# Performance work log

Measured on AMD Instinct MI355X. Metric: run time of the kernel, lower is better.

## Reference

```python
import jax, jax.numpy as jnp
import numpy as np

NEG = -1e20
EPS = float(np.finfo(np.float32).eps)


def setup_inputs() -> dict:
    key = jax.random.key(0)
    k1, k2, k3, k4 = jax.random.split(key, 4)
    B, S, E, D = 8, 2048, 1024, 1024
    return {
        "embeddings": jax.random.normal(k1, (B, S, E), dtype=jnp.float32),
        "mask": jnp.ones((B, S), dtype=jnp.int32),
        "W_q": jax.random.normal(k2, (E, D), dtype=jnp.float32),
        "W_k": jax.random.normal(k3, (E, D), dtype=jnp.float32),
        "W_v": jax.random.normal(k4, (E, D), dtype=jnp.float32),
    }


def reference(embeddings, mask, W_q, W_k, W_v):
    # embeddings: [B,S,E]; mask: [B,S] (1 = keep, 0 = pad)
    q = embeddings @ W_q            # [B,S,D]
    k = embeddings @ W_k            # [B,S,D]
    v = embeddings @ W_v            # [B,S,Dv]
    energy = jnp.einsum("bqd,bkd->bqk", q, k)  # [B,S,S]
    S = embeddings.shape[1]
    causal = jnp.tril(jnp.ones((S, S), dtype=bool))          # [S,S]
    energy = jnp.where(causal[None, :, :], energy, NEG)
    pad = (mask == 0)[:, None, :]                             # [B,1,S]
    energy = jnp.where(pad, NEG, energy)
    d_k = jnp.float32(W_k.shape[1])
    scale = jnp.sqrt(d_k) + EPS
    attention = jax.nn.softmax(energy / scale, axis=-1)       # [B,S,S]
    output = jnp.einsum("bqk,bkd->bqd", attention, v)         # [B,S,Dv]
    return output, attention
```

## Files before the change

kernel.cpp:

```cpp
#include <hip/hip_runtime.h>

#define Bb 8
#define Ss 2048
#define Ee 1024
#define Dd 1024

typedef __attribute__((ext_vector_type(8))) __bf16 bf16x8;
typedef __attribute__((ext_vector_type(4))) float f32x4;
typedef unsigned short u16;

__device__ __forceinline__ u16 f2bf(float x) {
  unsigned u = __float_as_uint(x);
  return (u16)((u + 0x7fffu + ((u >> 16) & 1u)) >> 16);
}
__device__ __forceinline__ float bf2f(u16 h) {
  return __uint_as_float(((unsigned)h) << 16);
}

__device__ __forceinline__ void gload16(const void* g, void* l) {
  __builtin_amdgcn_global_load_lds(
      (__attribute__((address_space(1))) void*)const_cast<void*>(g),
      (__attribute__((address_space(3))) void*)l, 16, 0, 0);
}

#define MFMA_BF16 __builtin_amdgcn_mfma_f32_16x16x32_bf16

__global__ __launch_bounds__(256) void k_split4(const float* __restrict__ in,
                                                u16* __restrict__ hi,
                                                u16* __restrict__ lo,
                                                long long n4) {
  long long i = (long long)blockIdx.x * 256 + threadIdx.x;
  if (i >= n4) return;
  float4 v = ((const float4*)in)[i];
  float xs[4] = {v.x, v.y, v.z, v.w};
  u16 hh[4], ll[4];
#pragma unroll
  for (int j = 0; j < 4; ++j) {
    hh[j] = f2bf(xs[j]);
    ll[j] = f2bf(xs[j] - bf2f(hh[j]));
  }
  ushort4 h, l;
  h.x = hh[0]; h.y = hh[1]; h.z = hh[2]; h.w = hh[3];
  l.x = ll[0]; l.y = ll[1]; l.z = ll[2]; l.w = ll[3];
  ((ushort4*)hi)[i] = h;
  ((ushort4*)lo)[i] = l;
}

__global__ __launch_bounds__(256) void k_wt_split(const float* __restrict__ W,
                                                  u16* __restrict__ hi,
                                                  u16* __restrict__ lo) {
  __shared__ float t[32][33];
  const int tx = threadIdx.x & 31;
  const int ty = threadIdx.x >> 5;
  const int e0 = blockIdx.y * 32, d0 = blockIdx.x * 32;
#pragma unroll
  for (int r = ty; r < 32; r += 8)
    t[r][tx] = W[(long long)(e0 + r) * Dd + d0 + tx];
  __syncthreads();
#pragma unroll
  for (int r = ty; r < 32; r += 8) {
    float x = t[tx][r];
    long long o = (long long)(d0 + r) * Ee + e0 + tx;
    u16 h = f2bf(x);
    hi[o] = h;
    if (lo) lo[o] = f2bf(x - bf2f(h));
  }
}

template <int EPI, bool CAUSAL>
__global__ __launch_bounds__(512, 4) void k_g128(
    const u16* __restrict__ Ah, const u16* __restrict__ Al,
    const u16* __restrict__ Bh, const u16* __restrict__ Bl,
    float* __restrict__ Cf, u16* __restrict__ Ch, u16* __restrict__ Cl,
    int nbx, int N, int K, long long strOp, long long strC) {
  const int nwg = gridDim.x;
  const int f = blockIdx.x;
  const int wgid = (f & 7) * (nwg >> 3) + (f >> 3);
  int bx, by, bz;
  if (CAUSAL) {
    bz = wgid / 136;
    const int t = wgid % 136;
    int yy = 0, c = 0;
    while (c + yy + 1 <= t) { c += yy + 1; ++yy; }
    by = yy;
    bx = t - c;
  } else {
    bz = 0;
    bx = wgid % nbx;
    by = wgid / nbx;
  }

  __shared__ __align__(16) u16 lds[2][4][4096];

  const int tid = threadIdx.x;
  const int lane = tid & 63;
  const int w = tid >> 6;
  const int wr = w >> 1;
  const int wc = w & 1;

  const long long ob = (long long)bz * strOp;
  const u16* srcBase[4] = {Ah + ob, Al + ob, Bh + ob, Bl + ob};
  const long long row0[2] = {(long long)by * 128, (long long)bx * 128};

  const int rL = tid >> 2;
  const int colOff = ((tid & 3) ^ ((tid >> 3) & 3)) * 8;
  const int rdOff = (lane & 15) * 64 + ((((lane >> 4) & 3) ^ ((lane >> 1) & 3)) << 4);

  const int AR = wr * 32;
  const int BR = wc * 64;
  const int nt = K / 32;

  const u16* gp[4];
#pragma unroll
  for (int m = 0; m < 4; ++m)
    gp[m] = srcBase[m] + (row0[m >> 1] + rL) * (long long)K + colOff;

#define STG(BUF)                                                       \
  {                                                                    \
    _Pragma("unroll") for (int m = 0; m < 4; ++m) {                    \
      gload16(gp[m], (char*)&lds[BUF][m][0] + tid * 16);               \
      gp[m] += 32;                                                     \
    }                                                                  \
  }
#define LDFRAG(MAT, R) \
  (*(const bf16x8*)((const char*)&lds[cur][MAT][0] + (R)*64 + rdOff))
#define BAR __builtin_amdgcn_s_barrier()

#define CLUSTER(NH)                                                          \
  __builtin_amdgcn_s_setprio(1);                                             \
  _Pragma("unroll") for (int m = 0; m < 2; ++m)                              \
      _Pragma("unroll") for (int n = 0; n < 2; ++n)                          \
          acc[m][(NH)*2 + n] =                                               \
      MFMA_BF16(aH[m], bL[n], acc[m][(NH)*2 + n], 0, 0, 0);                  \
  _Pragma("unroll") for (int m = 0; m < 2; ++m)                              \
      _Pragma("unroll") for (int n = 0; n < 2; ++n)                          \
          acc[m][(NH)*2 + n] =                                               \
      MFMA_BF16(aL[m], bH[n], acc[m][(NH)*2 + n], 0, 0, 0);                  \
  _Pragma("unroll") for (int m = 0; m < 2; ++m)                              \
      _Pragma("unroll") for (int n = 0; n < 2; ++n)                          \
          acc[m][(NH)*2 + n] =                                               \
      MFMA_BF16(aH[m], bH[n], acc[m][(NH)*2 + n], 0, 0, 0);                  \
  __builtin_amdgcn_s_setprio(0);

  f32x4 acc[2][4];
#pragma unroll
  for (int m = 0; m < 2; ++m)
#pragma unroll
    for (int n = 0; n < 4; ++n) acc[m][n] = f32x4{0.f, 0.f, 0.f, 0.f};

  bf16x8 aH[2], aL[2], bH[2], bL[2];

  STG(0);

  for (int kt = 0; kt < nt; ++kt) {
    const int cur = kt & 1;
    const bool more = (kt + 1 < nt);

    if (more) {
      STG(cur ^ 1);
      asm volatile("s_waitcnt vmcnt(4)" ::: "memory");
    } else {
      asm volatile("s_waitcnt vmcnt(0)" ::: "memory");
    }
    BAR;

#pragma unroll
    for (int m = 0; m < 2; ++m) {
      aH[m] = LDFRAG(0, AR + m * 16);
      aL[m] = LDFRAG(1, AR + m * 16);
    }
#pragma unroll
    for (int n = 0; n < 2; ++n) {
      bH[n] = LDFRAG(2, BR + n * 16);
      bL[n] = LDFRAG(3, BR + n * 16);
    }
    BAR;
    CLUSTER(0);
    BAR;

#pragma unroll
    for (int n = 0; n < 2; ++n) {
      bH[n] = LDFRAG(2, BR + 32 + n * 16);
      bL[n] = LDFRAG(3, BR + 32 + n * 16);
    }
    BAR;
    CLUSTER(1);
    BAR;
  }

  const int cr = (lane >> 4) << 2;
  const int cc = lane & 15;
#pragma unroll
  for (int m = 0; m < 2; ++m)
#pragma unroll
    for (int n = 0; n < 4; ++n)
#pragma unroll
      for (int r = 0; r < 4; ++r) {
        const long long row = (long long)by * 128 + wr * 32 + m * 16 + cr + r;
        const long long col = (long long)bx * 128 + wc * 64 + n * 16 + cc;
        const float v = acc[m][n][r];
        if constexpr (EPI == 0) {
          Cf[(long long)bz * strC + row * N + col] = v;
        } else {
          const long long idx = row * N + col;
          u16 h = f2bf(v);
          Ch[idx] = h;
          Cl[idx] = f2bf(v - bf2f(h));
        }
      }
#undef STG
#undef LDFRAG
#undef BAR
#undef CLUSTER
}

template <int EPI, bool TRIK>
__global__ __launch_bounds__(256) void k_gemm_bt(
    const u16* __restrict__ Ah, const u16* __restrict__ Bh,
    float* __restrict__ Cf, u16* __restrict__ Ch,
    int M, int N, int K, long long strA, long long strB, long long strC) {
  const int bx = blockIdx.x, by = blockIdx.y, bz = blockIdx.z;

  const int tid = threadIdx.x;
  const int lane = tid & 63;
  const int w = tid >> 6;
  const int wr = w >> 1, wc = w & 1;

  const u16* pAh = Ah + (long long)bz * strA;
  const u16* pBh = Bh + (long long)bz * strB;

  __shared__ __align__(16) u16 lds[2 * 128 * 32];
  char* ldsc = (char*)lds;

  const int srow = tid >> 2;
  const int scol = (tid & 3) * 8;
  const long long arow = (long long)by * 128 + srow;
  const long long brow = (long long)bx * 128 + srow;

  int ktEnd = K / 32;
  if (TRIK) {
    int lim = ((by + 1) * 128) / 32;
    if (lim < ktEnd) ktEnd = lim;
  }

  f32x4 acc[4][4];
#pragma unroll
  for (int i = 0; i < 4; ++i)
#pragma unroll
    for (int j = 0; j < 4; ++j) acc[i][j] = f32x4{0.f, 0.f, 0.f, 0.f};

  for (int kt = 0; kt < ktEnd; ++kt) {
    const int k0 = kt * 32 + scol;
    __syncthreads();
    gload16(pAh + arow * K + k0, ldsc + 0 * 4096 + w * 1024);
    gload16(pAh + (arow + 64) * K + k0, ldsc + 1 * 4096 + w * 1024);
    gload16(pBh + brow * K + k0, ldsc + 8192 + 0 * 4096 + w * 1024);
    gload16(pBh + (brow + 64) * K + k0, ldsc + 8192 + 1 * 4096 + w * 1024);
    __syncthreads();

    const int kk = (lane >> 4) * 8;
    const int ar = wr * 64 + (lane & 15);
    const int br = wc * 64 + (lane & 15);
    bf16x8 avh[4], bvh[4];
#pragma unroll
    for (int m = 0; m < 4; ++m)
      avh[m] = *(const bf16x8*)(lds + (ar + m * 16) * 32 + kk);
#pragma unroll
    for (int n = 0; n < 4; ++n)
      bvh[n] = *(const bf16x8*)(lds + 128 * 32 + (br + n * 16) * 32 + kk);
#pragma unroll
    for (int m = 0; m < 4; ++m)
#pragma unroll
      for (int n = 0; n < 4; ++n)
        acc[m][n] = MFMA_BF16(avh[m], bvh[n], acc[m][n], 0, 0, 0);
  }

  const int cr = wr * 64 + ((lane >> 4) << 2);
  const int cc = wc * 64 + (lane & 15);
  const long long rb = (long long)by * 128 + cr;
  const long long cb = (long long)bx * 128 + cc;
#pragma unroll
  for (int m = 0; m < 4; ++m)
#pragma unroll
    for (int n = 0; n < 4; ++n)
#pragma unroll
      for (int r = 0; r < 4; ++r) {
        const long long idx =
            (long long)bz * strC + (rb + m * 16 + r) * (long long)N + (cb + n * 16);
        const float v = acc[m][n][r];
        if constexpr (EPI == 0) Cf[idx] = v;
        else Ch[idx] = f2bf(v);
      }
}

__global__ __launch_bounds__(256) void k_softmax(float* __restrict__ attn,
                                                 u16* __restrict__ attn_bf,
                                                 const int* __restrict__ mask,
                                                 float inv_scale) {
  const int q = blockIdx.x;
  const int b = blockIdx.y;
  const int tid = threadIdx.x;
  float* row = attn + ((long long)b * Ss + q) * Ss;
  u16* rowb = attn_bf + ((long long)b * Ss + q) * Ss;
  const int* mrow = mask + b * Ss;
  const int qup = ((q >> 7) + 1) << 7;

  float x[8];
  float m = -3.0e38f;
#pragma unroll
  for (int j = 0; j < 8; ++j) {
    const int k = tid + j * 256;
    float v = -3.0e38f;
    if (k <= q) {
      const float e = row[k];
      v = ((mrow[k] != 0) ? e : -1e20f) * inv_scale;
    }
    x[j] = v;
    m = fmaxf(m, v);
  }
#pragma unroll
  for (int o = 32; o > 0; o >>= 1) m = fmaxf(m, __shfl_xor(m, o));
  __shared__ float redm[4], reds[4];
  const int w = tid >> 6;
  if ((tid & 63) == 0) redm[w] = m;
  __syncthreads();
  m = fmaxf(fmaxf(redm[0], redm[1]), fmaxf(redm[2], redm[3]));
  float s = 0.f;
#pragma unroll
  for (int j = 0; j < 8; ++j) {
    x[j] = __expf(x[j] - m);
    s += x[j];
  }
#pragma unroll
  for (int o = 32; o > 0; o >>= 1) s += __shfl_xor(s, o);
  if ((tid & 63) == 0) reds[w] = s;
  __syncthreads();
  s = reds[0] + reds[1] + reds[2] + reds[3];
  const float inv = 1.0f / s;
#pragma unroll
  for (int j = 0; j < 8; ++j) {
    const int k = tid + j * 256;
    if (k <= q) {
      const float a = x[j] * inv;
      row[k] = a;
      rowb[k] = f2bf(a);
    } else {
      row[k] = 0.0f;
      if (k < qup) rowb[k] = 0;
    }
  }
}

extern "C" void kernel_launch(void* const* d_in, const int* in_sizes, int n_in,
                              void* d_out, int out_size, void* d_ws, size_t ws_size,
                              hipStream_t stream) {
  const float* emb = (const float*)d_in[0];
  const int* mask = (const int*)d_in[1];
  const float* Wq = (const float*)d_in[2];
  const float* Wk = (const float*)d_in[3];
  const float* Wv = (const float*)d_in[4];

  float* out = (float*)d_out;
  float* attn = out + (long long)Bb * Ss * Dd;

  char* p = (char*)d_ws;
  u16* emb_hi = (u16*)p;
  u16* emb_lo = emb_hi + 16777216LL;
  u16* R_hi = (u16*)(p + 67108864LL);
  u16* R_lo = R_hi + 16777216LL;
  u16* v_t = R_lo + 16777216LL;
  u16* attn_bf = v_t + 16777216LL;
  u16* Wqr_hi = attn_bf + 16777216LL;
  u16* Wqr_lo = Wqr_hi + 1048576LL;
  u16* Wkr_hi = Wqr_lo + 1048576LL;
  u16* Wkr_lo = Wkr_hi + 1048576LL;
  u16* M_hi = Wkr_lo + 1048576LL;
  u16* M_lo = M_hi + 1048576LL;
  u16* WvT_hi = M_lo + 1048576LL;

  const float inv_scale = 1.0f / (32.0f + 1.1920929e-07f);

  k_split4<<<16384, 256, 0, stream>>>(emb, emb_hi, emb_lo, 4194304LL);
  k_split4<<<1024, 256, 0, stream>>>(Wq, Wqr_hi, Wqr_lo, 262144LL);
  k_split4<<<1024, 256, 0, stream>>>(Wk, Wkr_hi, Wkr_lo, 262144LL);
  k_wt_split<<<dim3(32, 32), 256, 0, stream>>>(Wv, WvT_hi, nullptr);

  k_g128<1, false><<<64, 512, 0, stream>>>(
      Wkr_hi, Wkr_lo, Wqr_hi, Wqr_lo, nullptr, M_hi, M_lo, 8, 1024, 1024, 0, 0);
  k_g128<1, false><<<1024, 512, 0, stream>>>(
      emb_hi, emb_lo, M_hi, M_lo, nullptr, R_hi, R_lo, 8, 1024, 1024, 0, 0);
  k_gemm_bt<2, false><<<dim3(16, 8, 8), 256, 0, stream>>>(
      WvT_hi, emb_hi, nullptr, v_t,
      1024, 2048, 1024, 0, (long long)Ss * Ee, (long long)Dd * Ss);
  k_g128<0, true><<<1088, 512, 0, stream>>>(
      R_hi, R_lo, emb_hi, emb_lo, attn, nullptr, nullptr,
      0, Ss, Dd, (long long)Ss * Dd, (long long)Ss * Ss);
  k_softmax<<<dim3(Ss, Bb), 256, 0, stream>>>(attn, attn_bf, mask, inv_scale);
  k_gemm_bt<0, true><<<dim3(8, 16, 8), 256, 0, stream>>>(
      attn_bf, v_t, out, nullptr,
      2048, 1024, 2048, (long long)Ss * Ss, (long long)Dd * Ss, (long long)Ss * Dd);
}
```

Baseline: 486.8 us.

## Replace simple bf16 GEMM with double-buffered 512-thread tile kernel for V and PV

Generalizes the double-buffered 128x128 tile kernel with a single-precision-pass mode: two bf16 operands instead of hi/lo pairs, optional batching through blockIdx.y, and triangular K limiting. It replaces the old 256-thread GEMM, which reloaded LDS behind two full barriers every K step with no prefetch, for the V projection and the attention-times-V product. The goal is to overlap global-to-LDS loads with MFMA work and to gain from the swizzled block ordering. The trade-off is a smaller per-wave output tile (32x64) and more barriers per iteration in the new path.

```diff
diff --git a/kernel.cpp b/kernel.cpp
--- a/kernel.cpp
+++ b/kernel.cpp
@@ -67,12 +67,13 @@
   }
 }
 
-template <int EPI, bool CAUSAL>
-__global__ __launch_bounds__(512, 4) void k_g128(
+template <int NP, int EPI, bool CAUSAL, bool TRIK>
+__global__ __launch_bounds__(512, 4) void k_t128(
     const u16* __restrict__ Ah, const u16* __restrict__ Al,
     const u16* __restrict__ Bh, const u16* __restrict__ Bl,
     float* __restrict__ Cf, u16* __restrict__ Ch, u16* __restrict__ Cl,
-    int nbx, int N, int K, long long strOp, long long strC) {
+    int nbx, int N, int K, long long strA, long long strB, long long strC) {
+  constexpr int NMAT = (NP == 3) ? 4 : 2;
   const int nwg = gridDim.x;
   const int f = blockIdx.x;
   const int wgid = (f & 7) * (nwg >> 3) + (f >> 3);
@@ -85,12 +86,12 @@
     by = yy;
     bx = t - c;
   } else {
-    bz = 0;
+    bz = blockIdx.y;
     bx = wgid % nbx;
     by = wgid / nbx;
   }
 
-  __shared__ __align__(16) u16 lds[2][4][4096];
+  __shared__ __align__(16) u16 lds[2][NMAT][4096];
 
   const int tid = threadIdx.x;
   const int lane = tid & 63;
@@ -98,8 +99,16 @@
   const int wr = w >> 1;
   const int wc = w & 1;
 
-  const long long ob = (long long)bz * strOp;
-  const u16* srcBase[4] = {Ah + ob, Al + ob, Bh + ob, Bl + ob};
+  const u16* srcBase[NMAT];
+  if constexpr (NP == 3) {
+    srcBase[0] = Ah + (long long)bz * strA;
+    srcBase[1] = Al + (long long)bz * strA;
+    srcBase[2] = Bh + (long long)bz * strB;
+    srcBase[3] = Bl + (long long)bz * strB;
+  } else {
+    srcBase[0] = Ah + (long long)bz * strA;
+    srcBase[1] = Bh + (long long)bz * strB;
+  }
   const long long row0[2] = {(long long)by * 128, (long long)bx * 128};
 
   const int rL = tid >> 2;
@@ -108,16 +117,22 @@
 
   const int AR = wr * 32;
   const int BR = wc * 64;
-  const int nt = K / 32;
-
-  const u16* gp[4];
-#pragma unroll
-  for (int m = 0; m < 4; ++m)
-    gp[m] = srcBase[m] + (row0[m >> 1] + rL) * (long long)K + colOff;
+  int nt = K / 32;
+  if (TRIK) {
+    const int lim = ((by + 1) * 128) / 32;
+    if (lim < nt) nt = lim;
+  }
+
+  const u16* gp[NMAT];
+#pragma unroll
+  for (int m = 0; m < NMAT; ++m) {
+    const int opsel = (NP == 3) ? (m >> 1) : m;
+    gp[m] = srcBase[m] + (row0[opsel] + rL) * (long long)K + colOff;
+  }
 
 #define STG(BUF)                                                       \
   {                                                                    \
-    _Pragma("unroll") for (int m = 0; m < 4; ++m) {                    \
+    _Pragma("unroll") for (int m = 0; m < NMAT; ++m) {                 \
       gload16(gp[m], (char*)&lds[BUF][m][0] + tid * 16);               \
       gp[m] += 32;                                                     \
     }                                                                  \
@@ -126,7 +141,7 @@
   (*(const bf16x8*)((const char*)&lds[cur][MAT][0] + (R)*64 + rdOff))
 #define BAR __builtin_amdgcn_s_barrier()
 
-#define CLUSTER(NH)                                                          \
+#define CLUSTER3(NH)                                                         \
   __builtin_amdgcn_s_setprio(1);                                             \
   _Pragma("unroll") for (int m = 0; m < 2; ++m)                              \
       _Pragma("unroll") for (int n = 0; n < 2; ++n)                          \
@@ -149,6 +164,7 @@
     for (int n = 0; n < 4; ++n) acc[m][n] = f32x4{0.f, 0.f, 0.f, 0.f};
 
   bf16x8 aH[2], aL[2], bH[2], bL[2];
+  bf16x8 bF[4];
 
   STG(0);
 
@@ -158,34 +174,52 @@
 
     if (more) {
       STG(cur ^ 1);
-      asm volatile("s_waitcnt vmcnt(4)" ::: "memory");
+      if constexpr (NP == 3)
+        asm volatile("s_waitcnt vmcnt(4)" ::: "memory");
+      else
+        asm volatile("s_waitcnt vmcnt(2)" ::: "memory");
     } else {
       asm volatile("s_waitcnt vmcnt(0)" ::: "memory");
     }
     BAR;
 
-#pragma unroll
-    for (int m = 0; m < 2; ++m) {
-      aH[m] = LDFRAG(0, AR + m * 16);
-      aL[m] = LDFRAG(1, AR + m * 16);
+    if constexpr (NP == 3) {
+#pragma unroll
+      for (int m = 0; m < 2; ++m) {
+        aH[m] = LDFRAG(0, AR + m * 16);
+        aL[m] = LDFRAG(1, AR + m * 16);
+      }
+#pragma unroll
+      for (int n = 0; n < 2; ++n) {
+        bH[n] = LDFRAG(2, BR + n * 16);
+        bL[n] = LDFRAG(3, BR + n * 16);
+      }
+      BAR;
+      CLUSTER3(0);
+      BAR;
+#pragma unroll
+      for (int n = 0; n < 2; ++n) {
+        bH[n] = LDFRAG(2, BR + 32 + n * 16);
+        bL[n] = LDFRAG(3, BR + 32 + n * 16);
+      }
+      BAR;
+      CLUSTER3(1);
+      BAR;
+    } else {
+#pragma unroll
+      for (int m = 0; m < 2; ++m) aH[m] = LDFRAG(0, AR + m * 16);
+#pragma unroll
+      for (int n = 0; n < 4; ++n) bF[n] = LDFRAG(1, BR + n * 16);
+      BAR;
+      __builtin_amdgcn_s_setprio(1);
+#pragma unroll
+      for (int m = 0; m < 2; ++m)
+#pragma unroll
+        for (int n = 0; n < 4; ++n)
+          acc[m][n] = MFMA_BF16(aH[m], bF[n], acc[m][n], 0, 0, 0);
+      __builtin_amdgcn_s_setprio(0);
+      BAR;
     }
-#pragma unroll
-    for (int n = 0; n < 2; ++n) {
-      bH[n] = LDFRAG(2, BR + n * 16);
-      bL[n] = LDFRAG(3, BR + n * 16);
-    }
-    BAR;
-    CLUSTER(0);
-    BAR;
-
-#pragma unroll
-    for (int n = 0; n < 2; ++n) {
-      bH[n] = LDFRAG(2, BR + 32 + n * 16);
-      bL[n] = LDFRAG(3, BR + 32 + n * 16);
-    }
-    BAR;
-    CLUSTER(1);
-    BAR;
   }
 
   const int cr = (lane >> 4) << 2;
@@ -201,96 +235,19 @@
         const float v = acc[m][n][r];
         if constexpr (EPI == 0) {
           Cf[(long long)bz * strC + row * N + col] = v;
-        } else {
+        } else if constexpr (EPI == 1) {
           const long long idx = row * N + col;
           u16 h = f2bf(v);
           Ch[idx] = h;
           Cl[idx] = f2bf(v - bf2f(h));
+        } else {
+          Ch[(long long)bz * strC + row * N + col] = f2bf(v);
         }
       }
 #undef STG
 #undef LDFRAG
 #undef BAR
-#undef CLUSTER
-}
-
-template <int EPI, bool TRIK>
-__global__ __launch_bounds__(256) void k_gemm_bt(
-    const u16* __restrict__ Ah, const u16* __restrict__ Bh,
-    float* __restrict__ Cf, u16* __restrict__ Ch,
-    int M, int N, int K, long long strA, long long strB, long long strC) {
-  const int bx = blockIdx.x, by = blockIdx.y, bz = blockIdx.z;
-
-  const int tid = threadIdx.x;
-  const int lane = tid & 63;
-  const int w = tid >> 6;
-  const int wr = w >> 1, wc = w & 1;
-
-  const u16* pAh = Ah + (long long)bz * strA;
-  const u16* pBh = Bh + (long long)bz * strB;
-
-  __shared__ __align__(16) u16 lds[2 * 128 * 32];
-  char* ldsc = (char*)lds;
-
-  const int srow = tid >> 2;
-  const int scol = (tid & 3) * 8;
-  const long long arow = (long long)by * 128 + srow;
-  const long long brow = (long long)bx * 128 + srow;
-
-  int ktEnd = K / 32;
-  if (TRIK) {
-    int lim = ((by + 1) * 128) / 32;
-    if (lim < ktEnd) ktEnd = lim;
-  }
-
-  f32x4 acc[4][4];
-#pragma unroll
-  for (int i = 0; i < 4; ++i)
-#pragma unroll
-    for (int j = 0; j < 4; ++j) acc[i][j] = f32x4{0.f, 0.f, 0.f, 0.f};
-
-  for (int kt = 0; kt < ktEnd; ++kt) {
-    const int k0 = kt * 32 + scol;
-    __syncthreads();
-    gload16(pAh + arow * K + k0, ldsc + 0 * 4096 + w * 1024);
-    gload16(pAh + (arow + 64) * K + k0, ldsc + 1 * 4096 + w * 1024);
-    gload16(pBh + brow * K + k0, ldsc + 8192 + 0 * 4096 + w * 1024);
-    gload16(pBh + (brow + 64) * K + k0, ldsc + 8192 + 1 * 4096 + w * 1024);
-    __syncthreads();
-
-    const int kk = (lane >> 4) * 8;
-    const int ar = wr * 64 + (lane & 15);
-    const int br = wc * 64 + (lane & 15);
-    bf16x8 avh[4], bvh[4];
-#pragma unroll
-    for (int m = 0; m < 4; ++m)
-      avh[m] = *(const bf16x8*)(lds + (ar + m * 16) * 32 + kk);
-#pragma unroll
-    for (int n = 0; n < 4; ++n)
-      bvh[n] = *(const bf16x8*)(lds + 128 * 32 + (br + n * 16) * 32 + kk);
-#pragma unroll
-    for (int m = 0; m < 4; ++m)
-#pragma unroll
-      for (int n = 0; n < 4; ++n)
-        acc[m][n] = MFMA_BF16(avh[m], bvh[n], acc[m][n], 0, 0, 0);
-  }
-
-  const int cr = wr * 64 + ((lane >> 4) << 2);
-  const int cc = wc * 64 + (lane & 15);
-  const long long rb = (long long)by * 128 + cr;
-  const long long cb = (long long)bx * 128 + cc;
-#pragma unroll
-  for (int m = 0; m < 4; ++m)
-#pragma unroll
-    for (int n = 0; n < 4; ++n)
-#pragma unroll
-      for (int r = 0; r < 4; ++r) {
-        const long long idx =
-            (long long)bz * strC + (rb + m * 16 + r) * (long long)N + (cb + n * 16);
-        const float v = acc[m][n][r];
-        if constexpr (EPI == 0) Cf[idx] = v;
-        else Ch[idx] = f2bf(v);
-      }
+#undef CLUSTER3
 }
 
 __global__ __launch_bounds__(256) void k_softmax(float* __restrict__ attn,
@@ -385,18 +342,20 @@
   k_split4<<<1024, 256, 0, stream>>>(Wk, Wkr_hi, Wkr_lo, 262144LL);
   k_wt_split<<<dim3(32, 32), 256, 0, stream>>>(Wv, WvT_hi, nullptr);
 
-  k_g128<1, false><<<64, 512, 0, stream>>>(
-      Wkr_hi, Wkr_lo, Wqr_hi, Wqr_lo, nullptr, M_hi, M_lo, 8, 1024, 1024, 0, 0);
-  k_g128<1, false><<<1024, 512, 0, stream>>>(
-      emb_hi, emb_lo, M_hi, M_lo, nullptr, R_hi, R_lo, 8, 1024, 1024, 0, 0);
-  k_gemm_bt<2, false><<<dim3(16, 8, 8), 256, 0, stream>>>(
-      WvT_hi, emb_hi, nullptr, v_t,
-      1024, 2048, 1024, 0, (long long)Ss * Ee, (long long)Dd * Ss);
-  k_g128<0, true><<<1088, 512, 0, stream>>>(
+  k_t128<3, 1, false, false><<<64, 512, 0, stream>>>(
+      Wkr_hi, Wkr_lo, Wqr_hi, Wqr_lo, nullptr, M_hi, M_lo,
+      8, 1024, 1024, 0, 0, 0);
+  k_t128<3, 1, false, false><<<1024, 512, 0, stream>>>(
+      emb_hi, emb_lo, M_hi, M_lo, nullptr, R_hi, R_lo,
+      8, 1024, 1024, 0, 0, 0);
+  k_t128<1, 2, false, false><<<dim3(128, 8), 512, 0, stream>>>(
+      WvT_hi, nullptr, emb_hi, nullptr, nullptr, v_t, nullptr,
+      16, Ss, Ee, 0, (long long)Ss * Ee, (long long)Dd * Ss);
+  k_t128<3, 0, true, false><<<1088, 512, 0, stream>>>(
       R_hi, R_lo, emb_hi, emb_lo, attn, nullptr, nullptr,
-      0, Ss, Dd, (long long)Ss * Dd, (long long)Ss * Ss);
+      0, Ss, Dd, (long long)Ss * Dd, (long long)Ss * Dd, (long long)Ss * Ss);
   k_softmax<<<dim3(Ss, Bb), 256, 0, stream>>>(attn, attn_bf, mask, inv_scale);
-  k_gemm_bt<0, true><<<dim3(8, 16, 8), 256, 0, stream>>>(
-      attn_bf, v_t, out, nullptr,
-      2048, 1024, 2048, (long long)Ss * Ss, (long long)Dd * Ss, (long long)Ss * Dd);
-}
+  k_t128<1, 0, false, true><<<dim3(128, 8), 512, 0, stream>>>(
+      attn_bf, nullptr, v_t, nullptr, out, nullptr, nullptr,
+      8, Dd, Ss, (long long)Ss * Ss, (long long)Dd * Ss, (long long)Ss * Dd);
+}
```

New measurement: 469.6 us. -3.5%, faster.
